# Kernel tuning notes

Hardware: AMD Instinct MI355X
Metric: run time of the kernel (lower is better)

The kernel has to match this reference:

```python
import jax, jax.numpy as jnp
import numpy as np

N, T, CIN, H, L, NC = 64, 150, 150, 1024, 3, 60
EPS = 1e-5


def setup_inputs() -> dict:
    key = jax.random.key(0)
    ks = jax.random.split(key, 12)
    s = 0.05
    return {
        "x": jax.random.normal(ks[0], (N, T, CIN), jnp.float32),
        "bn_gamma": jnp.ones((CIN,), jnp.float32),
        "bn_beta": jnp.zeros((CIN,), jnp.float32),
        "w_ih0": jax.random.normal(ks[1], (2, 3 * H, CIN), jnp.float32) * s,
        "w_hh0": jax.random.normal(ks[2], (2, 3 * H, H), jnp.float32) * s,
        "b_ih0": jax.random.normal(ks[3], (2, 3 * H), jnp.float32) * s,
        "b_hh0": jax.random.normal(ks[4], (2, 3 * H), jnp.float32) * s,
        "w_ih": jax.random.normal(ks[5], (L - 1, 2, 3 * H, 2 * H), jnp.float32) * s,
        "w_hh": jax.random.normal(ks[6], (L - 1, 2, 3 * H, H), jnp.float32) * s,
        "b_ih": jax.random.normal(ks[7], (L - 1, 2, 3 * H), jnp.float32) * s,
        "b_hh": jax.random.normal(ks[8], (L - 1, 2, 3 * H), jnp.float32) * s,
        "fc_w": jax.random.normal(ks[9], (NC, 2 * H), jnp.float32) * s,
        "fc_b": jax.random.normal(ks[10], (NC,), jnp.float32) * s,
    }


def _bigru_layer(x, w_ih, w_hh, b_ih, b_hh):
    # x: [T, N, I]. Faithful to the source's per-timestep loop: BOTH directions
    # scan forward in time (the 'reverse' direction never sees a reversed seq,
    # since the original feeds length-1 slices while carrying hidden state).
    # Precompute input projections for the whole sequence: [T, 2, N, 3H]
    gi = jnp.einsum('tni,dgi->tdng', x, w_ih) + b_ih[None, :, None, :]

    def step(h, gi_t):
        # h: [2, N, H], gi_t: [2, N, 3H]
        gh = jnp.einsum('dnh,dgh->dng', h, w_hh) + b_hh[:, None, :]
        r = jax.nn.sigmoid(gi_t[..., :H] + gh[..., :H])
        z = jax.nn.sigmoid(gi_t[..., H:2 * H] + gh[..., H:2 * H])
        n = jnp.tanh(gi_t[..., 2 * H:] + r * gh[..., 2 * H:])
        h_new = (1.0 - z) * n + z * h
        out = jnp.concatenate([h_new[0], h_new[1]], axis=-1)  # [N, 2H]
        return h_new, out

    h0 = jnp.zeros((2, x.shape[1], H), x.dtype)
    _, outs = jax.lax.scan(step, h0, gi)
    return outs  # [T, N, 2H]


def reference(x, bn_gamma, bn_beta, w_ih0, w_hh0, b_ih0, b_hh0,
              w_ih, w_hh, b_ih, b_hh, fc_w, fc_b):
    # BatchNorm1d over channels, train mode: batch stats over (N, T), biased var.
    mean = x.mean(axis=(0, 1))
    var = x.var(axis=(0, 1))
    xn = (x - mean) * jax.lax.rsqrt(var + EPS) * bn_gamma + bn_beta

    h = jnp.transpose(xn, (1, 0, 2))  # [T, N, CIN]
    h = _bigru_layer(h, w_ih0, w_hh0, b_ih0, b_hh0)
    for l in range(L - 1):  # small fixed layer loop
        h = _bigru_layer(h, w_ih[l], w_hh[l], b_ih[l], b_hh[l])

    # seq_len == T for every sample, so the gathered hidden is the last step.
    last = h[-1]  # [N, 2H]
    return last @ fc_w.T + fc_b  # [N, num_class]
```

## Files before the change

### kernel.cpp

```cpp
#include <hip/hip_runtime.h>
#include <math.h>

#define NB   64
#define TT   150
#define CIN  150
#define HH   1024
#define G3   3072
#define NCOL 6144
#define KP0  160
#define RT   9600
#define NC   60
#define NSLOT 151
#define SLOT_STRIDE 66560

using bf16x8 = __attribute__((ext_vector_type(8))) __bf16;
using f32x4  = __attribute__((ext_vector_type(4))) float;

static __device__ __forceinline__ unsigned short f2bf(float f){
  unsigned int x = __builtin_bit_cast(unsigned int, f);
  x += 0x7fffu + ((x >> 16) & 1u);
  return (unsigned short)(x >> 16);
}
static __device__ __forceinline__ float bf2f(unsigned short u){
  unsigned int x = ((unsigned int)u) << 16;
  return __builtin_bit_cast(float, x);
}
static __device__ __forceinline__ float sigmoidf(float x){
  return 1.0f / (1.0f + expf(-x));
}

static __device__ __forceinline__ void gload16(const void* g, void* l){
  __builtin_amdgcn_global_load_lds(
      (const __attribute__((address_space(1))) void*)g,
      (__attribute__((address_space(3))) void*)l, 16, 0, 0);
}

__global__ void bn_stats(const float* __restrict__ x, const float* __restrict__ gamma,
                         const float* __restrict__ beta, float* __restrict__ ss){
  const int c = blockIdx.x;
  float s = 0.f, s2 = 0.f;
  for (int i = threadIdx.x; i < RT; i += 256){
    float v = x[(size_t)i * CIN + c];
    s += v; s2 += v * v;
  }
  __shared__ float sh1[256], sh2[256];
  sh1[threadIdx.x] = s; sh2[threadIdx.x] = s2;
  __syncthreads();
  for (int st = 128; st > 0; st >>= 1){
    if ((int)threadIdx.x < st){
      sh1[threadIdx.x] += sh1[threadIdx.x + st];
      sh2[threadIdx.x] += sh2[threadIdx.x + st];
    }
    __syncthreads();
  }
  if (threadIdx.x == 0){
    float mean = sh1[0] * (1.f / RT);
    float var  = sh2[0] * (1.f / RT) - mean * mean;
    float sc   = rsqrtf(var + 1e-5f) * gamma[c];
    ss[c]       = sc;
    ss[CIN + c] = beta[c] - mean * sc;
  }
}

__global__ void bn_apply(const float* __restrict__ x, const float* __restrict__ ss,
                         unsigned short* __restrict__ xn){
  int idx = blockIdx.x * 256 + threadIdx.x;
  if (idx >= RT * KP0) return;
  int r = idx / KP0, c = idx - r * KP0;
  int t = r >> 6, n = r & 63;
  float v = 0.f;
  if (c < CIN) v = x[((size_t)n * TT + t) * CIN + c] * ss[c] + ss[CIN + c];
  xn[idx] = f2bf(v);
}

__global__ void cast_bf(const float* __restrict__ s, unsigned short* __restrict__ d, int n){
  for (int i = blockIdx.x * 256 + threadIdx.x; i < n; i += gridDim.x * 256)
    d[i] = f2bf(s[i]);
}

__global__ void cast_pad_w0(const float* __restrict__ w, unsigned short* __restrict__ d){
  int idx = blockIdx.x * 256 + threadIdx.x;
  if (idx >= NCOL * KP0) return;
  int row = idx / KP0, c = idx - row * KP0;
  d[idx] = (c < CIN) ? f2bf(w[(size_t)row * CIN + c]) : (unsigned short)0;
}

__global__ void zero16(uint4* p, int n){
  int i = blockIdx.x * 256 + threadIdx.x;
  if (i < n) p[i] = make_uint4(0u, 0u, 0u, 0u);
}

__global__ void guard_k(float* out){ out[0] = -12345.0f; }

__global__ __launch_bounds__(256) void gemm_tile(
    const unsigned short* __restrict__ A, const unsigned short* __restrict__ B,
    const float* __restrict__ bias, unsigned short* __restrict__ C, int K)
{
  const int r0 = blockIdx.x * 128;
  const int c0 = blockIdx.y * 128;
  const int tid = threadIdx.x;
  const int wid = tid >> 6;
  const int l   = tid & 63;
  const int lr  = l & 15;
  const int lk  = (l >> 4) * 8;
  const int wm  = wid >> 1;
  const int wn  = wid & 1;

  __shared__ unsigned short As[128 * 32];
  __shared__ unsigned short Bs[128 * 32];

  const int c1   = wid * 64 + l;
  const int rowS = c1 >> 2;
  const int ccS  = c1 & 3;

  f32x4 acc[4][4];
#pragma unroll
  for (int i = 0; i < 4; ++i)
#pragma unroll
    for (int j = 0; j < 4; ++j) acc[i][j] = f32x4{0,0,0,0};

  const unsigned short* Ag0 = A + (size_t)(r0 + rowS) * K + ccS * 8;
  const unsigned short* Ag1 = A + (size_t)(r0 + 64 + rowS) * K + ccS * 8;
  const unsigned short* Bg0 = B + (size_t)(c0 + rowS) * K + ccS * 8;
  const unsigned short* Bg1 = B + (size_t)(c0 + 64 + rowS) * K + ccS * 8;
  unsigned short* As0 = As + wid * 512;
  unsigned short* As1 = As + 2048 + wid * 512;
  unsigned short* Bs0 = Bs + wid * 512;
  unsigned short* Bs1 = Bs + 2048 + wid * 512;

  for (int k0 = 0; k0 < K; k0 += 32){
    gload16(Ag0 + k0, As0);
    gload16(Ag1 + k0, As1);
    gload16(Bg0 + k0, Bs0);
    gload16(Bg1 + k0, Bs1);
    __syncthreads();

    bf16x8 af[4], bfr[4];
#pragma unroll
    for (int mt = 0; mt < 4; ++mt)
      af[mt] = *(const bf16x8*)(As + (wm * 64 + mt * 16 + lr) * 32 + lk);
#pragma unroll
    for (int nt = 0; nt < 4; ++nt)
      bfr[nt] = *(const bf16x8*)(Bs + (wn * 64 + nt * 16 + lr) * 32 + lk);
#pragma unroll
    for (int mt = 0; mt < 4; ++mt)
#pragma unroll
      for (int nt = 0; nt < 4; ++nt)
        acc[mt][nt] = __builtin_amdgcn_mfma_f32_16x16x32_bf16(af[mt], bfr[nt], acc[mt][nt], 0, 0, 0);
    __syncthreads();
  }

  const int rb = (l >> 4) * 4;
#pragma unroll
  for (int mt = 0; mt < 4; ++mt){
#pragma unroll
    for (int nt = 0; nt < 4; ++nt){
      const int col = c0 + wn * 64 + nt * 16 + lr;
      const float bv = bias[col];
#pragma unroll
      for (int reg = 0; reg < 4; ++reg){
        const int row = r0 + wm * 64 + mt * 16 + rb + reg;
        C[(size_t)row * NCOL + col] = f2bf(acc[mt][nt][reg] + bv);
      }
    }
  }
}

__global__ __launch_bounds__(256, 1) void gru_layer(
    const unsigned short* __restrict__ whh,
    const float* __restrict__ bhh,
    const unsigned short* __restrict__ gi,
    unsigned short* __restrict__ outb,
    float* __restrict__ hfinal,
    unsigned short* __restrict__ hbig,
    int* __restrict__ flags, int wout)
{
  const int d  = blockIdx.x >> 6;
  const int jt = blockIdx.x & 63;
  const int j0 = jt * 16;
  const int w  = threadIdx.x >> 6;
  const int l  = threadIdx.x & 63;
  const int lr = l & 15;
  const int hi = l >> 4;

  __shared__ unsigned char wlds[98304];

  {
    const unsigned short* wsrc = whh + (size_t)d * (G3 * HH);
    for (int c = threadIdx.x; c < 6144; c += 256){
      int g   = c >> 11;
      int rem = c & 2047;
      int r   = rem >> 7;
      int kc  = rem & 127;
      uint4 v = *(const uint4*)(wsrc + (size_t)(g * HH + j0 + r) * HH + kc * 8);
      int kcs = (kc & ~7) | ((kc + r) & 7);
      *(uint4*)(wlds + g * 32768 + r * 2048 + kcs * 16) = v;
    }
  }
  __syncthreads();

  const float4 br4 = *(const float4*)(bhh + d * G3 +          j0 + hi * 4);
  const float4 bz4 = *(const float4*)(bhh + d * G3 + HH +     j0 + hi * 4);
  const float4 bn4 = *(const float4*)(bhh + d * G3 + 2 * HH + j0 + hi * 4);

  const int n    = w * 16 + lr;
  const int jcol = j0 + hi * 4;

  unsigned short* dirbase = hbig + (size_t)d * NSLOT * SLOT_STRIDE;

  float hold[4] = {0.f, 0.f, 0.f, 0.f};

  for (int t = 0; t < TT; ++t){
    const unsigned short* hprev = dirbase + (size_t)t * SLOT_STRIDE;
    unsigned short*       hnext = dirbase + (size_t)(t + 1) * SLOT_STRIDE;

    size_t gbase = (size_t)(t * NB + n) * NCOL + (size_t)d * G3 + jcol;
    ushort4 gr4 = *(const ushort4*)(gi + gbase);
    ushort4 gz4 = *(const ushort4*)(gi + gbase + HH);
    ushort4 gn4 = *(const ushort4*)(gi + gbase + 2 * HH);

    if (t){
      if (w == 0){
        const int* myfl = flags + d * 64;
        int cap = 0;
        for (;;){
          int f = __hip_atomic_load(&myfl[l], __ATOMIC_RELAXED, __HIP_MEMORY_SCOPE_AGENT);
          if (__all(f >= t)) break;
          if (++cap > 20000000) break;
          __builtin_amdgcn_s_sleep(1);
        }
      }
      __syncthreads();
    }

    f32x4 ar = {0,0,0,0}, az = {0,0,0,0}, an = {0,0,0,0};
    const unsigned short* hrow = hprev + (size_t)(w * 16 + lr) * HH + hi * 8;

#pragma unroll 8
    for (int k0 = 0; k0 < HH; k0 += 32){
      bf16x8 b = *(const bf16x8*)(hrow + k0);
      int kc  = (k0 >> 3) + hi;
      int kcs = (kc & ~7) | ((kc + lr) & 7);
      int off = lr * 2048 + kcs * 16;
      bf16x8 a_r = *(const bf16x8*)(wlds +          off);
      bf16x8 a_z = *(const bf16x8*)(wlds + 32768 +  off);
      bf16x8 a_n = *(const bf16x8*)(wlds + 65536 +  off);
      ar = __builtin_amdgcn_mfma_f32_16x16x32_bf16(a_r, b, ar, 0, 0, 0);
      az = __builtin_amdgcn_mfma_f32_16x16x32_bf16(a_z, b, az, 0, 0, 0);
      an = __builtin_amdgcn_mfma_f32_16x16x32_bf16(a_n, b, an, 0, 0, 0);
    }

    {
      ushort4 hb_;
      const float* br = (const float*)&br4;
      const float* bz = (const float*)&bz4;
      const float* bn_ = (const float*)&bn4;
      const unsigned short* g_r = (const unsigned short*)&gr4;
      const unsigned short* g_z = (const unsigned short*)&gz4;
      const unsigned short* g_n = (const unsigned short*)&gn4;
#pragma unroll
      for (int reg = 0; reg < 4; ++reg){
        float r  = sigmoidf(bf2f(g_r[reg]) + ar[reg] + br[reg]);
        float z  = sigmoidf(bf2f(g_z[reg]) + az[reg] + bz[reg]);
        float nn = tanhf(bf2f(g_n[reg]) + r * (an[reg] + bn_[reg]));
        hold[reg] = (1.f - z) * nn + z * hold[reg];
      }
      hb_.x = f2bf(hold[0]); hb_.y = f2bf(hold[1]);
      hb_.z = f2bf(hold[2]); hb_.w = f2bf(hold[3]);
      if (wout)
        *(ushort4*)(outb + (size_t)(t * NB + n) * (2 * HH) + (size_t)d * HH + jcol) = hb_;
      if (t == TT - 1)
        *(float4*)(hfinal + (size_t)(d * NB + n) * HH + jcol) =
            make_float4(hold[0], hold[1], hold[2], hold[3]);
      __hip_atomic_store((unsigned long long*)(hnext + (size_t)n * HH + jcol),
                         __builtin_bit_cast(unsigned long long, hb_),
                         __ATOMIC_RELAXED, __HIP_MEMORY_SCOPE_AGENT);
    }

    __syncthreads();
    if (threadIdx.x == 0)
      __hip_atomic_store(&flags[blockIdx.x], t + 1, __ATOMIC_RELEASE, __HIP_MEMORY_SCOPE_AGENT);
  }
}

__global__ void fc_kernel(const float* __restrict__ hf, const float* __restrict__ fw,
                          const float* __restrict__ fb, float* __restrict__ out){
  int b = blockIdx.x;
  int n = b / NC, c = b - n * NC;
  int l = threadIdx.x;
  float s = 0.f;
  for (int k = l; k < 2 * HH; k += 64){
    float hv = (k < HH) ? hf[(size_t)n * HH + k]
                        : hf[(size_t)(NB + n) * HH + (k - HH)];
    s += hv * fw[(size_t)c * (2 * HH) + k];
  }
#pragma unroll
  for (int off = 32; off > 0; off >>= 1) s += __shfl_down(s, off);
  if (l == 0) out[n * NC + c] = s + fb[c];
}

extern "C" void kernel_launch(void* const* d_in, const int* in_sizes, int n_in,
                              void* d_out, int out_size, void* d_ws, size_t ws_size,
                              hipStream_t stream)
{
  const float* x      = (const float*)d_in[0];
  const float* gamma  = (const float*)d_in[1];
  const float* beta   = (const float*)d_in[2];
  const float* w_ih0  = (const float*)d_in[3];
  const float* w_hh0  = (const float*)d_in[4];
  const float* b_ih0  = (const float*)d_in[5];
  const float* b_hh0  = (const float*)d_in[6];
  const float* w_ih   = (const float*)d_in[7];
  const float* w_hh   = (const float*)d_in[8];
  const float* b_ih   = (const float*)d_in[9];
  const float* b_hh   = (const float*)d_in[10];
  const float* fc_w   = (const float*)d_in[11];
  const float* fc_b   = (const float*)d_in[12];
  float* out = (float*)d_out;

  char* ws = (char*)d_ws;
  size_t off = 0;
  auto alloc = [&](size_t bytes)->void*{
    void* p = ws + off; off += (bytes + 255) & ~(size_t)255; return p;
  };
  unsigned short* whh_bf = (unsigned short*)alloc((size_t)3 * 2 * G3 * HH * 2);
  unsigned short* w0_bf  = (unsigned short*)alloc((size_t)NCOL * KP0 * 2);
  unsigned short* wih_bf = (unsigned short*)alloc((size_t)2 * NCOL * 2 * HH * 2);
  unsigned short* xn_bf  = (unsigned short*)alloc((size_t)RT * KP0 * 2);
  unsigned short* gi_bf  = (unsigned short*)alloc((size_t)RT * NCOL * 2);
  unsigned short* out0   = (unsigned short*)alloc((size_t)RT * 2 * HH * 2);
  unsigned short* out1   = (unsigned short*)alloc((size_t)RT * 2 * HH * 2);
  float* hfinal = (float*)alloc((size_t)2 * NB * HH * 4);
  unsigned short* hbig = (unsigned short*)alloc((size_t)2 * NSLOT * SLOT_STRIDE * 2);
  float* ss = (float*)alloc(2048);
  int* flags = (int*)alloc(1024);

  if (off > ws_size){ guard_k<<<1, 1, 0, stream>>>(out); return; }

  bn_stats<<<CIN, 256, 0, stream>>>(x, gamma, beta, ss);
  bn_apply<<<(RT * KP0 + 255) / 256, 256, 0, stream>>>(x, ss, xn_bf);
  cast_pad_w0<<<(NCOL * KP0 + 255) / 256, 256, 0, stream>>>(w_ih0, w0_bf);
  cast_bf<<<4096, 256, 0, stream>>>(w_hh0, whh_bf, 2 * G3 * HH);
  cast_bf<<<4096, 256, 0, stream>>>(w_hh,  whh_bf + (size_t)2 * G3 * HH, 2 * 2 * G3 * HH);
  cast_bf<<<4096, 256, 0, stream>>>(w_ih,  wih_bf, 2 * NCOL * 2 * HH);

  zero16<<<32, 256, 0, stream>>>((uint4*)hbig, NB * HH * 2 / 16);
  zero16<<<32, 256, 0, stream>>>((uint4*)(hbig + (size_t)NSLOT * SLOT_STRIDE),
                                 NB * HH * 2 / 16);

  for (int lyr = 0; lyr < 3; ++lyr){
    if (lyr == 0){
      gemm_tile<<<dim3(RT / 128, NCOL / 128), 256, 0, stream>>>(xn_bf, w0_bf, b_ih0, gi_bf, KP0);
    } else {
      const unsigned short* Ain = (lyr == 1) ? out0 : out1;
      gemm_tile<<<dim3(RT / 128, NCOL / 128), 256, 0, stream>>>(
          Ain, wih_bf + (size_t)(lyr - 1) * NCOL * 2 * HH,
          b_ih + (size_t)(lyr - 1) * NCOL, gi_bf, 2 * HH);
    }
    zero16<<<1, 32, 0, stream>>>((uint4*)flags, 512 / 16);

    const unsigned short* whh_l = whh_bf + (size_t)lyr * 2 * G3 * HH;
    const float* bhh_l = (lyr == 0) ? b_hh0 : (b_hh + (size_t)(lyr - 1) * NCOL);
    unsigned short* outb = (lyr == 0) ? out0 : out1;
    int wout = (lyr < 2) ? 1 : 0;
    gru_layer<<<128, 256, 0, stream>>>(whh_l, bhh_l, gi_bf, outb,
                                       hfinal, hbig, flags, wout);
  }
  fc_kernel<<<NB * NC, 64, 0, stream>>>(hfinal, fc_w, fc_b, out);
}
```

Baseline: 6.394 ms.

## Use a per-direction arrival counter and prefetch hidden-state chunks in GRU scan

Each block used to publish its own per-step flag, and wave 0 polled all 64 flags of its direction with a wave-wide vote. Now each block atomically increments one shared counter per direction, and a single thread spins until the counter reaches 64*t. The hidden-state loads feeding the MFMA loop are double-buffered in groups of eight so the next chunk's global loads overlap the current chunk's MFMAs. The store of the new hidden state is also moved ahead of the output writes so other blocks see it sooner. The cost is 64 contended atomics on one address per step and more vector registers held for the prefetch buffers.

```diff
diff --git a/kernel.cpp b/kernel.cpp
--- a/kernel.cpp
+++ b/kernel.cpp
@@ -207,6 +207,7 @@
   const int jcol = j0 + hi * 4;
 
   unsigned short* dirbase = hbig + (size_t)d * NSLOT * SLOT_STRIDE;
+  int* ctr = &flags[d * 64];
 
   float hold[4] = {0.f, 0.f, 0.f, 0.f};
 
@@ -220,14 +221,12 @@
     ushort4 gn4 = *(const ushort4*)(gi + gbase + 2 * HH);
 
     if (t){
-      if (w == 0){
-        const int* myfl = flags + d * 64;
+      if (threadIdx.x == 0){
+        const int tgt = 64 * t;
         int cap = 0;
-        for (;;){
-          int f = __hip_atomic_load(&myfl[l], __ATOMIC_RELAXED, __HIP_MEMORY_SCOPE_AGENT);
-          if (__all(f >= t)) break;
+        while (__hip_atomic_load(ctr, __ATOMIC_RELAXED, __HIP_MEMORY_SCOPE_AGENT) < tgt){
           if (++cap > 20000000) break;
-          __builtin_amdgcn_s_sleep(1);
+          __builtin_amdgcn_s_sleep(2);
         }
       }
       __syncthreads();
@@ -236,18 +235,34 @@
     f32x4 ar = {0,0,0,0}, az = {0,0,0,0}, an = {0,0,0,0};
     const unsigned short* hrow = hprev + (size_t)(w * 16 + lr) * HH + hi * 8;
 
-#pragma unroll 8
-    for (int k0 = 0; k0 < HH; k0 += 32){
-      bf16x8 b = *(const bf16x8*)(hrow + k0);
-      int kc  = (k0 >> 3) + hi;
-      int kcs = (kc & ~7) | ((kc + lr) & 7);
-      int off = lr * 2048 + kcs * 16;
-      bf16x8 a_r = *(const bf16x8*)(wlds +          off);
-      bf16x8 a_z = *(const bf16x8*)(wlds + 32768 +  off);
-      bf16x8 a_n = *(const bf16x8*)(wlds + 65536 +  off);
-      ar = __builtin_amdgcn_mfma_f32_16x16x32_bf16(a_r, b, ar, 0, 0, 0);
-      az = __builtin_amdgcn_mfma_f32_16x16x32_bf16(a_z, b, az, 0, 0, 0);
-      an = __builtin_amdgcn_mfma_f32_16x16x32_bf16(a_n, b, an, 0, 0, 0);
+    bf16x8 ha[8], hb[8];
+#pragma unroll
+    for (int i = 0; i < 8; ++i) ha[i] = *(const bf16x8*)(hrow + i * 32);
+
+#pragma unroll
+    for (int blk = 0; blk < 4; ++blk){
+      if (blk < 3){
+#pragma unroll
+        for (int i = 0; i < 8; ++i)
+          hb[i] = *(const bf16x8*)(hrow + (blk + 1) * 256 + i * 32);
+      }
+#pragma unroll
+      for (int i = 0; i < 8; ++i){
+        const int k0  = blk * 256 + i * 32;
+        const int kc  = (k0 >> 3) + hi;
+        const int kcs = (kc & ~7) | ((kc + lr) & 7);
+        const int off = lr * 2048 + kcs * 16;
+        bf16x8 a_r = *(const bf16x8*)(wlds +          off);
+        bf16x8 a_z = *(const bf16x8*)(wlds + 32768 +  off);
+        bf16x8 a_n = *(const bf16x8*)(wlds + 65536 +  off);
+        ar = __builtin_amdgcn_mfma_f32_16x16x32_bf16(a_r, ha[i], ar, 0, 0, 0);
+        az = __builtin_amdgcn_mfma_f32_16x16x32_bf16(a_z, ha[i], az, 0, 0, 0);
+        an = __builtin_amdgcn_mfma_f32_16x16x32_bf16(a_n, ha[i], an, 0, 0, 0);
+      }
+      if (blk < 3){
+#pragma unroll
+        for (int i = 0; i < 8; ++i) ha[i] = hb[i];
+      }
     }
 
     {
@@ -267,19 +282,19 @@
       }
       hb_.x = f2bf(hold[0]); hb_.y = f2bf(hold[1]);
       hb_.z = f2bf(hold[2]); hb_.w = f2bf(hold[3]);
+      __hip_atomic_store((unsigned long long*)(hnext + (size_t)n * HH + jcol),
+                         __builtin_bit_cast(unsigned long long, hb_),
+                         __ATOMIC_RELAXED, __HIP_MEMORY_SCOPE_AGENT);
       if (wout)
         *(ushort4*)(outb + (size_t)(t * NB + n) * (2 * HH) + (size_t)d * HH + jcol) = hb_;
       if (t == TT - 1)
         *(float4*)(hfinal + (size_t)(d * NB + n) * HH + jcol) =
             make_float4(hold[0], hold[1], hold[2], hold[3]);
-      __hip_atomic_store((unsigned long long*)(hnext + (size_t)n * HH + jcol),
-                         __builtin_bit_cast(unsigned long long, hb_),
-                         __ATOMIC_RELAXED, __HIP_MEMORY_SCOPE_AGENT);
     }
 
     __syncthreads();
     if (threadIdx.x == 0)
-      __hip_atomic_store(&flags[blockIdx.x], t + 1, __ATOMIC_RELEASE, __HIP_MEMORY_SCOPE_AGENT);
+      __hip_atomic_fetch_add(ctr, 1, __ATOMIC_RELEASE, __HIP_MEMORY_SCOPE_AGENT);
   }
 }
 
```

Result: no change. 6.390 ms (-0.1%).
